# Optimization experiments

Hardware: AMD Instinct MI355X
Metric: run time of the kernel (lower is better)

Reference implementation:

```python
import jax, jax.numpy as jnp
import numpy as np

EPS = 1e-8  # smoothing_radius


def setup_inputs() -> dict:
    key = jax.random.key(0)
    ks = jax.random.split(key, 8)
    T, S, D = 2048, 1024, 3
    H, FIN, FOUT = 64, 7, 4
    return {
        "reference_length": jnp.ones((), jnp.float32),
        "source_points": jax.random.normal(ks[0], (S, D), jnp.float32),
        "target_points": jax.random.normal(ks[1], (T, D), jnp.float32),
        "source_strengths": jax.random.uniform(ks[2], (S,), jnp.float32),
        "source_area": jax.random.uniform(ks[3], (S,), jnp.float32),
        "source_normal": jax.random.normal(ks[4], (S, D), jnp.float32),
        "W1": jax.random.normal(ks[5], (FIN, H), jnp.float32) / np.sqrt(FIN),
        "b1": jnp.zeros((H,), jnp.float32),
        "W2": jax.random.normal(ks[6], (H, FOUT), jnp.float32) / np.sqrt(H),
        "b2": jnp.zeros((FOUT,), jnp.float32),
    }


def _legendre4(x):
    # First 4 Legendre polynomials P1..P4 (n_spherical_harmonics = 4)
    x2 = x * x
    p1 = x
    p2 = 0.5 * (3.0 * x2 - 1.0)
    p3 = 0.5 * (5.0 * x2 - 3.0) * x
    p4 = 0.125 * ((35.0 * x2 - 30.0) * x2 + 3.0)
    return jnp.stack([p1, p2, p3, p4], axis=-1)


def _kernel_forward(reference_length, source_points, target_points,
                    source_strengths, source_area, source_normal,
                    W1, b1, W2, b2):
    D = source_points.shape[-1]
    # Dimensionless relative positions: [T, S, D]
    r = (target_points[:, None, :] - source_points[None, :, :]) / reference_length
    r2 = jnp.sum(r * r, axis=-1) + EPS * EPS          # [T, S]
    n2 = jnp.sum(source_normal * source_normal, -1) + EPS * EPS  # [S]
    # Invariant features: source scalar, smoothed log-magnitudes, pair Legendre terms
    log_r = 0.5 * jnp.log(r2)                          # [T, S]
    log_n = 0.5 * jnp.log(n2)                          # [S]
    cos = jnp.einsum('tsd,sd->ts', r, source_normal) / jnp.sqrt(r2 * n2[None, :])
    feats = jnp.concatenate([
        jnp.broadcast_to(source_area[None, :, None], r2.shape + (1,)),
        log_r[..., None],
        jnp.broadcast_to(log_n[None, :, None], r2.shape + (1,)),
        _legendre4(cos),
    ], axis=-1)                                        # [T, S, 7]
    # MLP kernel network with tanh squashing (network_type='mlp')
    h = jax.nn.silu(feats @ W1 + b1)                   # [T, S, 64]
    out = jnp.tanh(h @ W2 + b2)                        # [T, S, 4]
    # Physical far-field decay: scalar ~ 1/r^{D-2}, vector ~ 1/r^{D-1}
    inv_r = jax.lax.rsqrt(r2)
    decay_s = inv_r ** (D - 2)
    decay_v = inv_r ** (D - 1)
    w = source_strengths[None, :]                      # [1, S]
    scalar = jnp.sum(w * decay_s * out[..., 0], axis=-1)  # [T]
    # Rotationally invariant vector reprojection: radial + 2 coeffs per non-radial vector
    r_hat = r * inv_r[..., None]
    n_hat = source_normal / jnp.sqrt(n2)[:, None]
    n_hat_b = jnp.broadcast_to(n_hat[None], r.shape)
    vec = (out[..., 1:2] * r_hat
           + out[..., 2:3] * n_hat_b
           + out[..., 3:4] * jnp.cross(r_hat, n_hat_b))  # [T, S, D]
    vector = jnp.einsum('ts,tsd->td', w * decay_v, vec)   # [T, D]
    return jnp.concatenate([scalar[:, None], vector], axis=-1)  # [T, 1+D]


def reference(reference_length, source_points, target_points, source_strengths,
              source_area, source_normal, W1, b1, W2, b2):
    return _kernel_forward(reference_length, source_points, target_points,
                           source_strengths, source_area, source_normal,
                           W1, b1, W2, b2)
```

## Files before the change

### kernel.cpp

```cpp
#include <hip/hip_runtime.h>

typedef float v2f __attribute__((ext_vector_type(2)));

#define EPS2 1e-16f

constexpr int H     = 64;
constexpr int FIN   = 7;
constexpr int FOUT  = 4;
constexpr int BLOCK = 256;
constexpr int NCHUNK = 4;
constexpr int NV     = NCHUNK / 2;

__device__ __forceinline__ float rcpf_fast(float x) { return __builtin_amdgcn_rcpf(x); }
__device__ __forceinline__ float rsqf_fast(float x) { return __builtin_amdgcn_rsqf(x); }
__device__ __forceinline__ v2f splat(float x) { return v2f{x, x}; }
__device__ __forceinline__ v2f vfma(v2f a, v2f b, v2f c) { return __builtin_elementwise_fma(a, b, c); }

__device__ __forceinline__ float tanhf_fast(float x) {
    float cx = fminf(fmaxf(x, -15.0f), 15.0f);
    float e = __expf(2.0f * cx);
    return (e - 1.0f) * rcpf_fast(e + 1.0f);
}
__device__ __forceinline__ v2f tanhv(v2f x) {
    return v2f{tanhf_fast(x.x), tanhf_fast(x.y)};
}

__global__ __launch_bounds__(BLOCK, 2)
void bh_kernel(const float* __restrict__ refLenP,
               const float* __restrict__ srcP,
               const float* __restrict__ tgtP,
               const float* __restrict__ wgtP,
               const float* __restrict__ areaP,
               const float* __restrict__ srcN,
               const float* __restrict__ W1,
               const float* __restrict__ b1,
               const float* __restrict__ W2,
               const float* __restrict__ b2,
               float* __restrict__ out,
               int S)
{
    __shared__ float sW1t[H * 8];
    __shared__ float sW2[H * FOUT];
    __shared__ float red[4][4];

    const int tid = threadIdx.x;

    for (int i = tid; i < H * 8; i += BLOCK) {
        int h = i >> 3, f = i & 7;
        sW1t[i] = (f < FIN) ? W1[f * H + h] : b1[h];
    }
    for (int i = tid; i < H * FOUT; i += BLOCK) sW2[i] = W2[i];
    __syncthreads();

    const int t = blockIdx.x;
    const float invL = rcpf_fast(refLenP[0]);
    const float tx = tgtP[t * 3 + 0];
    const float ty = tgtP[t * 3 + 1];
    const float tz = tgtP[t * 3 + 2];

    v2f feats[NV][FIN];
    v2f ws_s[NV], wv_s[NV];
    v2f rhx[NV], rhy[NV], rhz[NV];
    v2f nhx[NV], nhy[NV], nhz[NV];

    #pragma unroll
    for (int v = 0; v < NV; ++v) {
        const int sA = tid + (2 * v) * BLOCK;
        const int sB = sA + BLOCK;
        const int cA = (sA < S) ? sA : (S - 1);
        const int cB = (sB < S) ? sB : (S - 1);
        const float wA = (sA < S) ? wgtP[cA] : 0.0f;
        const float wB = (sB < S) ? wgtP[cB] : 0.0f;

        v2f rx = v2f{(tx - srcP[cA * 3 + 0]) * invL, (tx - srcP[cB * 3 + 0]) * invL};
        v2f ry = v2f{(ty - srcP[cA * 3 + 1]) * invL, (ty - srcP[cB * 3 + 1]) * invL};
        v2f rz = v2f{(tz - srcP[cA * 3 + 2]) * invL, (tz - srcP[cB * 3 + 2]) * invL};
        v2f nx = v2f{srcN[cA * 3 + 0], srcN[cB * 3 + 0]};
        v2f ny = v2f{srcN[cA * 3 + 1], srcN[cB * 3 + 1]};
        v2f nz = v2f{srcN[cA * 3 + 2], srcN[cB * 3 + 2]};

        v2f r2 = vfma(rx, rx, vfma(ry, ry, rz * rz)) + splat(EPS2);
        v2f n2 = vfma(nx, nx, vfma(ny, ny, nz * nz)) + splat(EPS2);
        v2f inv_r = v2f{rsqf_fast(r2.x), rsqf_fast(r2.y)};
        v2f inv_n = v2f{rsqf_fast(n2.x), rsqf_fast(n2.y)};
        v2f log_r = v2f{__logf(r2.x), __logf(r2.y)} * splat(0.5f);
        v2f log_n = v2f{__logf(n2.x), __logf(n2.y)} * splat(0.5f);
        v2f cosv = vfma(rx, nx, vfma(ry, ny, rz * nz)) * inv_r * inv_n;
        v2f c2 = cosv * cosv;

        feats[v][0] = v2f{(sA < S) ? areaP[cA] : 0.0f, (sB < S) ? areaP[cB] : 0.0f};
        feats[v][1] = log_r;
        feats[v][2] = log_n;
        feats[v][3] = cosv;
        feats[v][4] = vfma(c2, splat(1.5f), splat(-0.5f));
        feats[v][5] = (c2 * splat(2.5f) - splat(1.5f)) * cosv;
        feats[v][6] = vfma(vfma(c2, splat(4.375f), splat(-3.75f)), c2, splat(0.375f));

        v2f w = v2f{wA, wB};
        ws_s[v] = w * inv_r;
        wv_s[v] = w * inv_r * inv_r;
        rhx[v] = rx * inv_r; rhy[v] = ry * inv_r; rhz[v] = rz * inv_r;
        nhx[v] = nx * inv_n; nhy[v] = ny * inv_n; nhz[v] = nz * inv_n;
    }

    v2f o0[NV], o1[NV], o2[NV], o3[NV];
    {
        const float bb0 = b2[0], bb1 = b2[1], bb2 = b2[2], bb3 = b2[3];
        #pragma unroll
        for (int v = 0; v < NV; ++v) {
            o0[v] = splat(bb0); o1[v] = splat(bb1);
            o2[v] = splat(bb2); o3[v] = splat(bb3);
        }
    }

    #pragma unroll 8
    for (int h = 0; h < H; ++h) {
        const float4 wa = *reinterpret_cast<const float4*>(&sW1t[h * 8]);
        const float4 wb = *reinterpret_cast<const float4*>(&sW1t[h * 8 + 4]);
        const float4 w2 = *reinterpret_cast<const float4*>(&sW2[h * 4]);
        #pragma unroll
        for (int v = 0; v < NV; ++v) {
            v2f a = splat(wb.w);
            a = vfma(feats[v][0], splat(wa.x), a);
            a = vfma(feats[v][1], splat(wa.y), a);
            a = vfma(feats[v][2], splat(wa.z), a);
            a = vfma(feats[v][3], splat(wa.w), a);
            a = vfma(feats[v][4], splat(wb.x), a);
            a = vfma(feats[v][5], splat(wb.y), a);
            a = vfma(feats[v][6], splat(wb.z), a);
            v2f e  = v2f{__expf(-a.x), __expf(-a.y)};
            v2f sg = v2f{rcpf_fast(1.0f + e.x), rcpf_fast(1.0f + e.y)};
            v2f hv = a * sg;
            o0[v] = vfma(hv, splat(w2.x), o0[v]);
            o1[v] = vfma(hv, splat(w2.y), o1[v]);
            o2[v] = vfma(hv, splat(w2.z), o2[v]);
            o3[v] = vfma(hv, splat(w2.w), o3[v]);
        }
    }

    v2f a0 = splat(0.0f), a1 = splat(0.0f), a2 = splat(0.0f), a3 = splat(0.0f);
    #pragma unroll
    for (int v = 0; v < NV; ++v) {
        v2f t0 = tanhv(o0[v]);
        v2f t1 = tanhv(o1[v]);
        v2f t2 = tanhv(o2[v]);
        v2f t3 = tanhv(o3[v]);
        a0 = vfma(ws_s[v], t0, a0);
        v2f cxx = rhy[v] * nhz[v] - rhz[v] * nhy[v];
        v2f cxy = rhz[v] * nhx[v] - rhx[v] * nhz[v];
        v2f cxz = rhx[v] * nhy[v] - rhy[v] * nhx[v];
        v2f vx = t1 * rhx[v] + t2 * nhx[v] + t3 * cxx;
        v2f vy = t1 * rhy[v] + t2 * nhy[v] + t3 * cxy;
        v2f vz = t1 * rhz[v] + t2 * nhz[v] + t3 * cxz;
        a1 = vfma(wv_s[v], vx, a1);
        a2 = vfma(wv_s[v], vy, a2);
        a3 = vfma(wv_s[v], vz, a3);
    }
    float acc0 = a0.x + a0.y;
    float acc1 = a1.x + a1.y;
    float acc2 = a2.x + a2.y;
    float acc3 = a3.x + a3.y;

    #pragma unroll
    for (int off = 32; off > 0; off >>= 1) {
        acc0 += __shfl_down(acc0, off);
        acc1 += __shfl_down(acc1, off);
        acc2 += __shfl_down(acc2, off);
        acc3 += __shfl_down(acc3, off);
    }
    const int wave = tid >> 6;
    const int lane = tid & 63;
    if (lane == 0) {
        red[wave][0] = acc0; red[wave][1] = acc1;
        red[wave][2] = acc2; red[wave][3] = acc3;
    }
    __syncthreads();
    if (tid < 4) {
        float v = red[0][tid] + red[1][tid] + red[2][tid] + red[3][tid];
        out[t * 4 + tid] = v;
    }
}

extern "C" void kernel_launch(void* const* d_in, const int* in_sizes, int n_in,
                              void* d_out, int out_size, void* d_ws, size_t ws_size,
                              hipStream_t stream) {
    const float* refLen = (const float*)d_in[0];
    const float* srcP   = (const float*)d_in[1];
    const float* tgtP   = (const float*)d_in[2];
    const float* w      = (const float*)d_in[3];
    const float* area   = (const float*)d_in[4];
    const float* srcN   = (const float*)d_in[5];
    const float* W1     = (const float*)d_in[6];
    const float* b1     = (const float*)d_in[7];
    const float* W2     = (const float*)d_in[8];
    const float* b2     = (const float*)d_in[9];
    float* out          = (float*)d_out;

    const int S = in_sizes[3];
    const int T = in_sizes[2] / 3;

    bh_kernel<<<T, BLOCK, 0, stream>>>(refLen, srcP, tgtP, w, area, srcN,
                                       W1, b1, W2, b2, out, S);
}
```

Measured before the change: 124.0 us.

## Pre-pack MLP weights in workspace and read via uniform global loads instead of LDS

A tiny pre-kernel packs W1, b1 and W2 into a 16-float-per-hidden-unit layout in the workspace. The main kernel then reads the weights straight from global memory with wave-uniform float4 loads, which the compiler may turn into scalar loads. This removes the per-block LDS staging loop and its __syncthreads. It also drops the occupancy hint from launch_bounds and lowers the inner unroll from 8 to 4. The cost is an extra kernel launch, and the weights now come through the cache hierarchy rather than from LDS.

```diff
diff --git a/kernel.cpp b/kernel.cpp
--- a/kernel.cpp
+++ b/kernel.cpp
@@ -6,7 +6,6 @@
 
 constexpr int H     = 64;
 constexpr int FIN   = 7;
-constexpr int FOUT  = 4;
 constexpr int BLOCK = 256;
 constexpr int NCHUNK = 4;
 constexpr int NV     = NCHUNK / 2;
@@ -25,33 +24,40 @@
     return v2f{tanhf_fast(x.x), tanhf_fast(x.y)};
 }
 
-__global__ __launch_bounds__(BLOCK, 2)
+__global__ void pack_weights(const float* __restrict__ W1,
+                             const float* __restrict__ b1,
+                             const float* __restrict__ W2,
+                             float* __restrict__ wpk)
+{
+    int h = threadIdx.x;
+    if (h < H) {
+        float* p = wpk + h * 16;
+        #pragma unroll
+        for (int f = 0; f < FIN; ++f) p[f] = W1[f * H + h];
+        p[7]  = b1[h];
+        p[8]  = W2[h * 4 + 0];
+        p[9]  = W2[h * 4 + 1];
+        p[10] = W2[h * 4 + 2];
+        p[11] = W2[h * 4 + 3];
+        p[12] = 0.f; p[13] = 0.f; p[14] = 0.f; p[15] = 0.f;
+    }
+}
+
+__global__ __launch_bounds__(BLOCK)
 void bh_kernel(const float* __restrict__ refLenP,
                const float* __restrict__ srcP,
                const float* __restrict__ tgtP,
                const float* __restrict__ wgtP,
                const float* __restrict__ areaP,
                const float* __restrict__ srcN,
-               const float* __restrict__ W1,
-               const float* __restrict__ b1,
-               const float* __restrict__ W2,
+               const float* __restrict__ wpk,
                const float* __restrict__ b2,
                float* __restrict__ out,
                int S)
 {
-    __shared__ float sW1t[H * 8];
-    __shared__ float sW2[H * FOUT];
     __shared__ float red[4][4];
 
     const int tid = threadIdx.x;
-
-    for (int i = tid; i < H * 8; i += BLOCK) {
-        int h = i >> 3, f = i & 7;
-        sW1t[i] = (f < FIN) ? W1[f * H + h] : b1[h];
-    }
-    for (int i = tid; i < H * FOUT; i += BLOCK) sW2[i] = W2[i];
-    __syncthreads();
-
     const int t = blockIdx.x;
     const float invL = rcpf_fast(refLenP[0]);
     const float tx = tgtP[t * 3 + 0];
@@ -113,11 +119,12 @@
         }
     }
 
-    #pragma unroll 8
+    const float4* wq = reinterpret_cast<const float4*>(wpk);
+    #pragma unroll 4
     for (int h = 0; h < H; ++h) {
-        const float4 wa = *reinterpret_cast<const float4*>(&sW1t[h * 8]);
-        const float4 wb = *reinterpret_cast<const float4*>(&sW1t[h * 8 + 4]);
-        const float4 w2 = *reinterpret_cast<const float4*>(&sW2[h * 4]);
+        const float4 wa = wq[h * 4 + 0];
+        const float4 wb = wq[h * 4 + 1];
+        const float4 w2 = wq[h * 4 + 2];
         #pragma unroll
         for (int v = 0; v < NV; ++v) {
             v2f a = splat(wb.w);
@@ -195,10 +202,12 @@
     const float* W2     = (const float*)d_in[8];
     const float* b2     = (const float*)d_in[9];
     float* out          = (float*)d_out;
+    float* wpk          = (float*)d_ws;
 
     const int S = in_sizes[3];
     const int T = in_sizes[2] / 3;
 
+    pack_weights<<<1, 64, 0, stream>>>(W1, b1, W2, wpk);
     bh_kernel<<<T, BLOCK, 0, stream>>>(refLen, srcP, tgtP, w, area, srcN,
-                                       W1, b1, W2, b2, out, S);
-}
+                                       wpk, b2, out, S);
+}
```

Measured after the change: 125.8 us. No clear change (+1.4%).
